# Performance work log

Measured on AMD Instinct MI355X. Metric: run time of the kernel, lower is better.

Reference implementation:

```python
import jax, jax.numpy as jnp
import numpy as np

N, C, H, W = 4, 128, 64, 64


def setup_inputs() -> dict:
    key = jax.random.key(0)
    ks = jax.random.split(key, 4)
    s = 1.0 / np.sqrt(C).astype(np.float32)  # conv2d default-init scale
    return {
        "x": jax.random.normal(ks[0], (N, C, H, W), dtype=jnp.float32),
        "Wq": jax.random.normal(ks[1], (C, C), dtype=jnp.float32) * s,
        "bq": jnp.zeros((C,), dtype=jnp.float32),
        "Wk": jax.random.normal(ks[2], (C, C), dtype=jnp.float32) * s,
        "bk": jnp.zeros((C,), dtype=jnp.float32),
        "Wv": jax.random.normal(ks[3], (C, C), dtype=jnp.float32) * s,
        "bv": jnp.zeros((C,), dtype=jnp.float32),
    }


def reference(x, Wq, bq, Wk, bk, Wv, bv):
    n, c, h, w = x.shape
    xf = x.reshape(n, c, h * w)  # [N, C, L], L = H*W
    # 1x1 convs == per-pixel channel mixing
    q = jnp.einsum('oc,ncl->nol', Wq, xf) + bq[:, None]
    k = jnp.einsum('oc,ncl->nol', Wk, xf) + bk[:, None]
    v = jnp.einsum('oc,ncl->nol', Wv, xf) + bv[:, None]
    # scores[l, m] = sum_c k[c,l] * q[c,m]  (matmul(k^T, q))
    scale = jnp.asarray(1.0 / np.sqrt(c), x.dtype)
    scores = jnp.einsum('ncl,ncm->nlm', k, q) * scale  # [N, L, L]
    temp = jax.nn.softmax(scores, axis=-1)
    attn = jnp.einsum('ncl,nlm->ncm', v, temp)  # [N, C, L]
    return x + attn.reshape(n, c, h, w)
```

## Files before the change

kernel.cpp:

```cpp
#include <hip/hip_runtime.h>
#include <hip/hip_bf16.h>
#include <stdint.h>

#define NB 4
#define CH 128
#define LL 4096

typedef __attribute__((ext_vector_type(8))) short short8;
typedef __attribute__((ext_vector_type(4))) short short4b;
typedef __attribute__((ext_vector_type(4))) float floatx4;
typedef __attribute__((ext_vector_type(16))) float floatx16;


static __device__ __forceinline__ short f2bf(float f) {
    uint32_t u = __float_as_uint(f);
    u += 0x7fffu + ((u >> 16) & 1u);
    return (short)(u >> 16);
}
static __device__ __forceinline__ float bf2f(short s) {
    return __uint_as_float(((uint32_t)(uint16_t)s) << 16);
}

__global__ __launch_bounds__(256) void wprep_kernel(
    const float* __restrict__ Wq, const float* __restrict__ Wk,
    const float* __restrict__ Wv, short* __restrict__ Wf)
{
    const int g = blockIdx.x * 256 + threadIdx.x;
    const int mat = g >> 14;
    const int rem = g & 16383;
    const int o   = rem >> 7;
    const int c   = rem & 127;
    const float* W = (mat == 0) ? Wq : (mat == 1) ? Wk : Wv;
    float v = W[o * CH + c];
    if (mat == 1) v *= 0.08838834764831845f;
    Wf[(size_t)mat * 16384 + (o >> 4) * 2048 + (c >> 5) * 512
       + ((c >> 3) & 3) * 128 + (o & 15) * 8 + (c & 7)] = f2bf(v);
}

__global__ __launch_bounds__(256) void proj_kernel(
    const float* __restrict__ x, const short* __restrict__ Wf,
    const float* __restrict__ bq, const float* __restrict__ bk,
    const float* __restrict__ bv,
    short* __restrict__ Qf, short* __restrict__ Kf, short* __restrict__ Vp)
{
    const int i    = blockIdx.x;
    const int n    = (i >> 1) & 3;
    const int lt   = ((i >> 3) << 1) | (i & 1);
    const int l0   = lt << 5;
    const int tid  = threadIdx.x;
    const int wave = tid >> 6;
    const int lane = tid & 63;
    const int quad = lane >> 4;
    const int mc   = lane & 15;

    __shared__ short Xb[32][136];

    {
        const int sl = tid & 31;
        const int cg = tid >> 5;
        const float* xp = x + ((size_t)n * CH + cg * 16) * LL + l0 + sl;
        short8 buf;
        #pragma unroll
        for (int i2 = 0; i2 < 16; ++i2) {
            buf[i2 & 7] = f2bf(xp[(size_t)i2 * LL]);
            if ((i2 & 7) == 7)
                *(short8*)(void*)&Xb[sl][cg * 16 + (i2 & 8)] = buf;
        }
    }
    __syncthreads();

    const int lt2 = wave >> 1;
    const int oh  = wave & 1;
    const int gt  = lt * 2 + lt2;

    short8 xf[4];
    #pragma unroll
    for (int s = 0; s < 4; ++s)
        xf[s] = *(const short8*)(const void*)&Xb[lt2 * 16 + mc][32 * s + quad * 8];

    const size_t obase = ((size_t)n * 256 + gt) * 2048;
    const float scale = 0.08838834764831845f;

    #pragma unroll
    for (int mat = 0; mat < 3; ++mat) {
        const short* Wm = Wf + (size_t)mat * 16384;
        const float* bb = (mat == 0) ? bq : (mat == 1) ? bk : bv;
        const float bscale = (mat == 1) ? scale : 1.0f;
        #pragma unroll
        for (int ot = oh * 4; ot < oh * 4 + 4; ++ot) {
            floatx4 acc = {0.f, 0.f, 0.f, 0.f};
            #pragma unroll
            for (int s = 0; s < 4; ++s)
                acc = __builtin_amdgcn_mfma_f32_16x16x32_bf16(
                    *(const short8*)(const void*)(Wm + ot * 2048 + s * 512 + lane * 8),
                    xf[s], acc, 0, 0, 0);
            const int c0 = ot * 16 + 4 * quad;
            if (mat < 2) {
                short4b pv;
                #pragma unroll
                for (int r = 0; r < 4; ++r)
                    pv[r] = f2bf(acc[r] + bb[c0 + r] * bscale);
                short* dst = ((mat == 0) ? Qf : Kf) + obase
                           + (c0 >> 5) * 512 + ((c0 >> 3) & 3) * 128
                           + mc * 8 + (c0 & 7);
                *(short4b*)(void*)dst = pv;
            } else {
                #pragma unroll
                for (int r = 0; r < 4; ++r)
                    Vp[obase + (c0 + r) * 16 + mc] = f2bf(acc[r] + bb[c0 + r]);
            }
        }
    }
}

__global__ __launch_bounds__(1024) void rowsum_kernel(
    const short* __restrict__ Qf, const short* __restrict__ Kf,
    float* __restrict__ Dv)
{
    const int i    = blockIdx.x;
    const int n    = (i >> 1) & 3;
    const int tq   = ((i >> 3) << 1) | (i & 1);
    const int tid  = threadIdx.x;
    const int wave = tid >> 6;
    const int lane = tid & 63;
    const int quad = lane >> 4;
    const int mc   = lane & 15;
    const int mw   = wave & 7;
    const int th   = wave >> 3;

    __shared__ float Db[16][32];

    const short* Kb = Kf + ((size_t)n * 256 + tq * 4 + th * 2) * 2048 + lane * 8;
    short8 kf[2][4];
    #pragma unroll
    for (int t = 0; t < 2; ++t)
        #pragma unroll
        for (int s = 0; s < 4; ++s)
            kf[t][s] = *(const short8*)(const void*)(Kb + t * 2048 + s * 512);

    const short* Qn = Qf + (size_t)n * 524288 + (size_t)mw * 32 * 2048 + lane * 8;
    float rs[2][4] = {{0.f, 0.f, 0.f, 0.f}, {0.f, 0.f, 0.f, 0.f}};

    for (int it = 0; it < 32; ++it) {
        short8 q[4];
        #pragma unroll
        for (int s = 0; s < 4; ++s)
            q[s] = *(const short8*)(const void*)(
                Qn + (size_t)it * 2048 + s * 512);
        floatx4 a0 = {0.f, 0.f, 0.f, 0.f};
        floatx4 a1 = {0.f, 0.f, 0.f, 0.f};
        #pragma unroll
        for (int s = 0; s < 4; ++s) {
            a0 = __builtin_amdgcn_mfma_f32_16x16x32_bf16(kf[0][s], q[s], a0, 0, 0, 0);
            a1 = __builtin_amdgcn_mfma_f32_16x16x32_bf16(kf[1][s], q[s], a1, 0, 0, 0);
        }
        #pragma unroll
        for (int r = 0; r < 4; ++r) {
            rs[0][r] += __expf(a0[r]);
            rs[1][r] += __expf(a1[r]);
        }
    }

    #pragma unroll
    for (int t = 0; t < 2; ++t)
        #pragma unroll
        for (int r = 0; r < 4; ++r) {
            float v = rs[t][r];
            v += __shfl_xor(v, 1);
            v += __shfl_xor(v, 2);
            v += __shfl_xor(v, 4);
            v += __shfl_xor(v, 8);
            if (mc == 0) Db[wave][t * 16 + quad * 4 + r] = v;
        }
    __syncthreads();
    if (tid < 64) {
        const int lh = tid >> 5, lr = tid & 31;
        float s = 0.f;
        #pragma unroll
        for (int m = 0; m < 8; ++m) s += Db[lh * 8 + m][lr];
        Dv[(size_t)n * 4096 + tq * 64 + tid] = 1.0f / s;
    }
}

__global__ __launch_bounds__(512, 4) void attn_out_kernel(
    const short* __restrict__ Qf, const short* __restrict__ Kf,
    const short* __restrict__ Vp, const float* __restrict__ Dv,
    float* __restrict__ Po)
{
    const int i    = blockIdx.x;
    const int n    = (i >> 1) & 3;
    const int j    = ((i >> 3) << 1) | (i & 1);
    const int lh   = j >> 6;
    const int mb   = j & 63;
    const int m0   = mb << 6;
    const int tid  = threadIdx.x;
    const int wave = tid >> 6;
    const int lane = tid & 63;
    const int quad = lane >> 4;
    const int mc   = lane & 15;
    const int l32  = lane & 31;
    const int h    = lane >> 5;
    const int ct   = wave & 3;
    const int mh   = wave >> 2;

    __shared__ short P[2][64][260];

    const short* Qn  = Qf + (size_t)n * 524288;
    const short* Kn  = Kf + (size_t)n * 524288;
    const short* Vpn = Vp + (size_t)n * 524288;
    const float* Dn  = Dv + (size_t)n * 4096;
    const int tile0  = lh * 128;

    floatx16 acc;
    #pragma unroll
    for (int r = 0; r < 16; ++r) acc[r] = 0.f;

    for (int t = 0; t < 8; ++t) {
        const int p = t & 1;

        {
            const int tb = tile0 + t * 16 + 2 * wave;
            short8 kfr[2][4];
            #pragma unroll
            for (int jj = 0; jj < 2; ++jj)
                #pragma unroll
                for (int s = 0; s < 4; ++s)
                    kfr[jj][s] = *(const short8*)(const void*)(
                        Kn + (size_t)(tb + jj) * 2048 + s * 512 + lane * 8);
            floatx4 dr[2];
            #pragma unroll
            for (int jj = 0; jj < 2; ++jj)
                dr[jj] = *(const floatx4*)(const void*)(
                    Dn + (tb + jj) * 16 + quad * 4);

            #pragma unroll
            for (int mst = 0; mst < 4; ++mst) {
                short8 qt[4];
                #pragma unroll
                for (int s = 0; s < 4; ++s)
                    qt[s] = *(const short8*)(const void*)(
                        Qn + (size_t)((m0 >> 4) + mst) * 2048 + s * 512 + lane * 8);
                floatx4 sa0 = {0.f, 0.f, 0.f, 0.f};
                floatx4 sa1 = {0.f, 0.f, 0.f, 0.f};
                #pragma unroll
                for (int s = 0; s < 4; ++s) {
                    sa0 = __builtin_amdgcn_mfma_f32_16x16x32_bf16(kfr[0][s], qt[s], sa0, 0, 0, 0);
                    sa1 = __builtin_amdgcn_mfma_f32_16x16x32_bf16(kfr[1][s], qt[s], sa1, 0, 0, 0);
                }
                short4b pv0, pv1;
                #pragma unroll
                for (int r = 0; r < 4; ++r) {
                    pv0[r] = f2bf(__expf(sa0[r]) * dr[0][r]);
                    pv1[r] = f2bf(__expf(sa1[r]) * dr[1][r]);
                }
                *(short4b*)(void*)&P[p][16 * mst + mc][32 * wave + quad * 4] = pv0;
                *(short4b*)(void*)&P[p][16 * mst + mc][32 * wave + 16 + quad * 4] = pv1;
            }
        }
        __syncthreads();

        #pragma unroll
        for (int kc = 0; kc < 16; ++kc) {
            const short8 vf = *(const short8*)(const void*)(
                Vpn + (size_t)(tile0 + t * 16 + kc) * 2048
                    + (32 * ct + l32) * 16 + 8 * h);
            const short8 pf = *(const short8*)(const void*)&P[p][32 * mh + l32][16 * kc + 8 * h];
            acc = __builtin_amdgcn_mfma_f32_32x32x16_bf16(vf, pf, acc, 0, 0, 0);
        }
    }

    float* Pon = Po + (size_t)(lh * 4 + n) * 524288;
    #pragma unroll
    for (int r = 0; r < 16; ++r) {
        const int c = 32 * ct + (r & 3) + 8 * (r >> 2) + 4 * h;
        const int m = m0 + 32 * mh + l32;
        Pon[(size_t)c * LL + m] = acc[r];
    }
}

__global__ __launch_bounds__(256) void combine_kernel(
    const float* __restrict__ x, const float* __restrict__ Po,
    float* __restrict__ out)
{
    const size_t k = (size_t)blockIdx.x * 256 + threadIdx.x;
    const floatx4 a = *(const floatx4*)(const void*)(x + 4 * k);
    const floatx4 b = *(const floatx4*)(const void*)(Po + 4 * k);
    const floatx4 c = *(const floatx4*)(const void*)(Po + 2097152 + 4 * k);
    floatx4 o;
    #pragma unroll
    for (int r = 0; r < 4; ++r) o[r] = a[r] + b[r] + c[r];
    *(floatx4*)(void*)(out + 4 * k) = o;
}

extern "C" void kernel_launch(void* const* d_in, const int* in_sizes, int n_in,
                              void* d_out, int out_size, void* d_ws, size_t ws_size,
                              hipStream_t stream) {
    (void)in_sizes; (void)n_in; (void)out_size; (void)ws_size;
    const float* x  = (const float*)d_in[0];
    const float* Wq = (const float*)d_in[1];
    const float* bq = (const float*)d_in[2];
    const float* Wk = (const float*)d_in[3];
    const float* bk = (const float*)d_in[4];
    const float* Wv = (const float*)d_in[5];
    const float* bv = (const float*)d_in[6];
    float* out = (float*)d_out;

    char* ws = (char*)d_ws;
    short* Qf = (short*)(ws);
    short* Kf = (short*)(ws + 4194304);
    short* Vp = (short*)(ws + 8388608);
    float* Dv = (float*)(ws + 12582912);
    short* Wf = (short*)(ws + 16777216);
    float* Po = (float*)(ws + 16908288);

    wprep_kernel<<<192, 256, 0, stream>>>(Wq, Wk, Wv, Wf);
    proj_kernel<<<512, 256, 0, stream>>>(x, Wf, bq, bk, bv, Qf, Kf, Vp);
    rowsum_kernel<<<256, 1024, 0, stream>>>(Qf, Kf, Dv);
    attn_out_kernel<<<512, 512, 0, stream>>>(Qf, Kf, Vp, Dv, Po);
    combine_kernel<<<2048, 256, 0, stream>>>(x, Po, out);
}
```

Before: 179.2 us.

## Fuse all stages into one cooperative persistent kernel with grid syncs

```diff
diff --git a/kernel.cpp b/kernel.cpp
--- a/kernel.cpp
+++ b/kernel.cpp
@@ -1,6 +1,9 @@
 #include <hip/hip_runtime.h>
 #include <hip/hip_bf16.h>
+#include <hip/hip_cooperative_groups.h>
 #include <stdint.h>
+
+namespace cg = cooperative_groups;
 
 #define NB 4
 #define CH 128
@@ -17,182 +20,26 @@
     u += 0x7fffu + ((u >> 16) & 1u);
     return (short)(u >> 16);
 }
-static __device__ __forceinline__ float bf2f(short s) {
-    return __uint_as_float(((uint32_t)(uint16_t)s) << 16);
-}
-
-__global__ __launch_bounds__(256) void wprep_kernel(
-    const float* __restrict__ Wq, const float* __restrict__ Wk,
-    const float* __restrict__ Wv, short* __restrict__ Wf)
+
+__global__ __launch_bounds__(1024) void mega_kernel(
+    const float* __restrict__ x,
+    const float* __restrict__ Wq, const float* __restrict__ bq,
+    const float* __restrict__ Wk, const float* __restrict__ bk,
+    const float* __restrict__ Wv, const float* __restrict__ bv,
+    short* __restrict__ Qf, short* __restrict__ Kf, short* __restrict__ Vp,
+    float* __restrict__ Dv, short* __restrict__ Wf,
+    float* __restrict__ out)
 {
-    const int g = blockIdx.x * 256 + threadIdx.x;
-    const int mat = g >> 14;
-    const int rem = g & 16383;
-    const int o   = rem >> 7;
-    const int c   = rem & 127;
-    const float* W = (mat == 0) ? Wq : (mat == 1) ? Wk : Wv;
-    float v = W[o * CH + c];
-    if (mat == 1) v *= 0.08838834764831845f;
-    Wf[(size_t)mat * 16384 + (o >> 4) * 2048 + (c >> 5) * 512
-       + ((c >> 3) & 3) * 128 + (o & 15) * 8 + (c & 7)] = f2bf(v);
-}
-
-__global__ __launch_bounds__(256) void proj_kernel(
-    const float* __restrict__ x, const short* __restrict__ Wf,
-    const float* __restrict__ bq, const float* __restrict__ bk,
-    const float* __restrict__ bv,
-    short* __restrict__ Qf, short* __restrict__ Kf, short* __restrict__ Vp)
-{
-    const int i    = blockIdx.x;
-    const int n    = (i >> 1) & 3;
-    const int lt   = ((i >> 3) << 1) | (i & 1);
-    const int l0   = lt << 5;
-    const int tid  = threadIdx.x;
-    const int wave = tid >> 6;
-    const int lane = tid & 63;
-    const int quad = lane >> 4;
-    const int mc   = lane & 15;
-
-    __shared__ short Xb[32][136];
-
-    {
-        const int sl = tid & 31;
-        const int cg = tid >> 5;
-        const float* xp = x + ((size_t)n * CH + cg * 16) * LL + l0 + sl;
-        short8 buf;
-        #pragma unroll
-        for (int i2 = 0; i2 < 16; ++i2) {
-            buf[i2 & 7] = f2bf(xp[(size_t)i2 * LL]);
-            if ((i2 & 7) == 7)
-                *(short8*)(void*)&Xb[sl][cg * 16 + (i2 & 8)] = buf;
-        }
-    }
-    __syncthreads();
-
-    const int lt2 = wave >> 1;
-    const int oh  = wave & 1;
-    const int gt  = lt * 2 + lt2;
-
-    short8 xf[4];
-    #pragma unroll
-    for (int s = 0; s < 4; ++s)
-        xf[s] = *(const short8*)(const void*)&Xb[lt2 * 16 + mc][32 * s + quad * 8];
-
-    const size_t obase = ((size_t)n * 256 + gt) * 2048;
-    const float scale = 0.08838834764831845f;
-
-    #pragma unroll
-    for (int mat = 0; mat < 3; ++mat) {
-        const short* Wm = Wf + (size_t)mat * 16384;
-        const float* bb = (mat == 0) ? bq : (mat == 1) ? bk : bv;
-        const float bscale = (mat == 1) ? scale : 1.0f;
-        #pragma unroll
-        for (int ot = oh * 4; ot < oh * 4 + 4; ++ot) {
-            floatx4 acc = {0.f, 0.f, 0.f, 0.f};
-            #pragma unroll
-            for (int s = 0; s < 4; ++s)
-                acc = __builtin_amdgcn_mfma_f32_16x16x32_bf16(
-                    *(const short8*)(const void*)(Wm + ot * 2048 + s * 512 + lane * 8),
-                    xf[s], acc, 0, 0, 0);
-            const int c0 = ot * 16 + 4 * quad;
-            if (mat < 2) {
-                short4b pv;
-                #pragma unroll
-                for (int r = 0; r < 4; ++r)
-                    pv[r] = f2bf(acc[r] + bb[c0 + r] * bscale);
-                short* dst = ((mat == 0) ? Qf : Kf) + obase
-                           + (c0 >> 5) * 512 + ((c0 >> 3) & 3) * 128
-                           + mc * 8 + (c0 & 7);
-                *(short4b*)(void*)dst = pv;
-            } else {
-                #pragma unroll
-                for (int r = 0; r < 4; ++r)
-                    Vp[obase + (c0 + r) * 16 + mc] = f2bf(acc[r] + bb[c0 + r]);
-            }
-        }
-    }
-}
-
-__global__ __launch_bounds__(1024) void rowsum_kernel(
-    const short* __restrict__ Qf, const short* __restrict__ Kf,
-    float* __restrict__ Dv)
-{
-    const int i    = blockIdx.x;
-    const int n    = (i >> 1) & 3;
-    const int tq   = ((i >> 3) << 1) | (i & 1);
-    const int tid  = threadIdx.x;
-    const int wave = tid >> 6;
-    const int lane = tid & 63;
-    const int quad = lane >> 4;
-    const int mc   = lane & 15;
-    const int mw   = wave & 7;
-    const int th   = wave >> 3;
-
-    __shared__ float Db[16][32];
-
-    const short* Kb = Kf + ((size_t)n * 256 + tq * 4 + th * 2) * 2048 + lane * 8;
-    short8 kf[2][4];
-    #pragma unroll
-    for (int t = 0; t < 2; ++t)
-        #pragma unroll
-        for (int s = 0; s < 4; ++s)
-            kf[t][s] = *(const short8*)(const void*)(Kb + t * 2048 + s * 512);
-
-    const short* Qn = Qf + (size_t)n * 524288 + (size_t)mw * 32 * 2048 + lane * 8;
-    float rs[2][4] = {{0.f, 0.f, 0.f, 0.f}, {0.f, 0.f, 0.f, 0.f}};
-
-    for (int it = 0; it < 32; ++it) {
-        short8 q[4];
-        #pragma unroll
-        for (int s = 0; s < 4; ++s)
-            q[s] = *(const short8*)(const void*)(
-                Qn + (size_t)it * 2048 + s * 512);
-        floatx4 a0 = {0.f, 0.f, 0.f, 0.f};
-        floatx4 a1 = {0.f, 0.f, 0.f, 0.f};
-        #pragma unroll
-        for (int s = 0; s < 4; ++s) {
-            a0 = __builtin_amdgcn_mfma_f32_16x16x32_bf16(kf[0][s], q[s], a0, 0, 0, 0);
-            a1 = __builtin_amdgcn_mfma_f32_16x16x32_bf16(kf[1][s], q[s], a1, 0, 0, 0);
-        }
-        #pragma unroll
-        for (int r = 0; r < 4; ++r) {
-            rs[0][r] += __expf(a0[r]);
-            rs[1][r] += __expf(a1[r]);
-        }
-    }
-
-    #pragma unroll
-    for (int t = 0; t < 2; ++t)
-        #pragma unroll
-        for (int r = 0; r < 4; ++r) {
-            float v = rs[t][r];
-            v += __shfl_xor(v, 1);
-            v += __shfl_xor(v, 2);
-            v += __shfl_xor(v, 4);
-            v += __shfl_xor(v, 8);
-            if (mc == 0) Db[wave][t * 16 + quad * 4 + r] = v;
-        }
-    __syncthreads();
-    if (tid < 64) {
-        const int lh = tid >> 5, lr = tid & 31;
-        float s = 0.f;
-        #pragma unroll
-        for (int m = 0; m < 8; ++m) s += Db[lh * 8 + m][lr];
-        Dv[(size_t)n * 4096 + tq * 64 + tid] = 1.0f / s;
-    }
-}
-
-__global__ __launch_bounds__(512, 4) void attn_out_kernel(
-    const short* __restrict__ Qf, const short* __restrict__ Kf,
-    const short* __restrict__ Vp, const float* __restrict__ Dv,
-    float* __restrict__ Po)
-{
-    const int i    = blockIdx.x;
-    const int n    = (i >> 1) & 3;
-    const int j    = ((i >> 3) << 1) | (i & 1);
-    const int lh   = j >> 6;
-    const int mb   = j & 63;
-    const int m0   = mb << 6;
+    cg::grid_group grid = cg::this_grid();
+
+    __shared__ union SH {
+        short P2[2][2][64][264];
+        short Xb[4][16][136];
+        float Db[16][32];
+        float Rb[8192];
+    } sh;
+
+    const int ib   = blockIdx.x;
     const int tid  = threadIdx.x;
     const int wave = tid >> 6;
     const int lane = tid & 63;
@@ -200,96 +47,235 @@
     const int mc   = lane & 15;
     const int l32  = lane & 31;
     const int h    = lane >> 5;
-    const int ct   = wave & 3;
-    const int mh   = wave >> 2;
-
-    __shared__ short P[2][64][260];
-
-    const short* Qn  = Qf + (size_t)n * 524288;
-    const short* Kn  = Kf + (size_t)n * 524288;
-    const short* Vpn = Vp + (size_t)n * 524288;
-    const float* Dn  = Dv + (size_t)n * 4096;
-    const int tile0  = lh * 128;
-
-    floatx16 acc;
-    #pragma unroll
-    for (int r = 0; r < 16; ++r) acc[r] = 0.f;
-
-    for (int t = 0; t < 8; ++t) {
-        const int p = t & 1;
+
+    const int n   = (ib >> 1) & 3;
+    const int b64 = ((ib >> 3) << 1) | (ib & 1);
+
+    {
+        const int g = ib * 1024 + tid;
+        if (g < 49152) {
+            const int mat = g >> 14;
+            const int rem = g & 16383;
+            const int o   = rem >> 7;
+            const int c   = rem & 127;
+            const float* W = (mat == 0) ? Wq : (mat == 1) ? Wk : Wv;
+            float v = W[o * CH + c];
+            if (mat == 1) v *= 0.08838834764831845f;
+            Wf[(size_t)mat * 16384 + (o >> 4) * 2048 + (c >> 5) * 512
+               + ((c >> 3) & 3) * 128 + (o & 15) * 8 + (c & 7)] = f2bf(v);
+        }
+    }
+    grid.sync();
+
+    {
+        const int sub  = tid >> 8;
+        const int stid = tid & 255;
+        const int gt   = b64 * 4 + sub;
+        const int l0   = gt << 4;
+        const int w4   = (tid >> 6) & 3;
 
         {
-            const int tb = tile0 + t * 16 + 2 * wave;
-            short8 kfr[2][4];
-            #pragma unroll
-            for (int jj = 0; jj < 2; ++jj)
+            const int sl = stid & 15;
+            const int cg = stid >> 4;
+            const float* xp = x + ((size_t)n * CH + cg * 8) * LL + l0 + sl;
+            short8 buf;
+            #pragma unroll
+            for (int i2 = 0; i2 < 8; ++i2)
+                buf[i2] = f2bf(xp[(size_t)i2 * LL]);
+            *(short8*)(void*)&sh.Xb[sub][sl][cg * 8] = buf;
+        }
+        __syncthreads();
+
+        short8 xf[4];
+        #pragma unroll
+        for (int s = 0; s < 4; ++s)
+            xf[s] = *(const short8*)(const void*)&sh.Xb[sub][mc][32 * s + quad * 8];
+
+        const size_t obase = ((size_t)n * 256 + gt) * 2048;
+        const float scale = 0.08838834764831845f;
+
+        #pragma unroll
+        for (int mat = 0; mat < 3; ++mat) {
+            const short* Wm = Wf + (size_t)mat * 16384;
+            const float* bb = (mat == 0) ? bq : (mat == 1) ? bk : bv;
+            const float bscale = (mat == 1) ? scale : 1.0f;
+            #pragma unroll
+            for (int oo = 0; oo < 2; ++oo) {
+                const int ot = w4 * 2 + oo;
+                floatx4 acc = {0.f, 0.f, 0.f, 0.f};
                 #pragma unroll
                 for (int s = 0; s < 4; ++s)
-                    kfr[jj][s] = *(const short8*)(const void*)(
-                        Kn + (size_t)(tb + jj) * 2048 + s * 512 + lane * 8);
-            floatx4 dr[2];
-            #pragma unroll
-            for (int jj = 0; jj < 2; ++jj)
-                dr[jj] = *(const floatx4*)(const void*)(
-                    Dn + (tb + jj) * 16 + quad * 4);
-
-            #pragma unroll
-            for (int mst = 0; mst < 4; ++mst) {
-                short8 qt[4];
+                    acc = __builtin_amdgcn_mfma_f32_16x16x32_bf16(
+                        *(const short8*)(const void*)(Wm + ot * 2048 + s * 512 + lane * 8),
+                        xf[s], acc, 0, 0, 0);
+                const int c0 = ot * 16 + 4 * quad;
+                if (mat < 2) {
+                    short4b pv;
+                    #pragma unroll
+                    for (int r = 0; r < 4; ++r)
+                        pv[r] = f2bf(acc[r] + bb[c0 + r] * bscale);
+                    short* dst = ((mat == 0) ? Qf : Kf) + obase
+                               + (c0 >> 5) * 512 + ((c0 >> 3) & 3) * 128
+                               + mc * 8 + (c0 & 7);
+                    *(short4b*)(void*)dst = pv;
+                } else {
+                    #pragma unroll
+                    for (int r = 0; r < 4; ++r)
+                        Vp[obase + (c0 + r) * 16 + mc] = f2bf(acc[r] + bb[c0 + r]);
+                }
+            }
+        }
+    }
+    grid.sync();
+
+    {
+        const int tq = b64;
+        const int mw = wave & 7;
+        const int th = wave >> 3;
+
+        const short* Kb = Kf + ((size_t)n * 256 + tq * 4 + th * 2) * 2048 + lane * 8;
+        short8 kf[2][4];
+        #pragma unroll
+        for (int t = 0; t < 2; ++t)
+            #pragma unroll
+            for (int s = 0; s < 4; ++s)
+                kf[t][s] = *(const short8*)(const void*)(Kb + t * 2048 + s * 512);
+
+        const short* Qn = Qf + (size_t)n * 524288 + (size_t)mw * 32 * 2048 + lane * 8;
+        float rs[2][4] = {{0.f, 0.f, 0.f, 0.f}, {0.f, 0.f, 0.f, 0.f}};
+
+        for (int it = 0; it < 32; ++it) {
+            short8 q[4];
+            #pragma unroll
+            for (int s = 0; s < 4; ++s)
+                q[s] = *(const short8*)(const void*)(Qn + (size_t)it * 2048 + s * 512);
+            floatx4 a0 = {0.f, 0.f, 0.f, 0.f};
+            floatx4 a1 = {0.f, 0.f, 0.f, 0.f};
+            #pragma unroll
+            for (int s = 0; s < 4; ++s) {
+                a0 = __builtin_amdgcn_mfma_f32_16x16x32_bf16(kf[0][s], q[s], a0, 0, 0, 0);
+                a1 = __builtin_amdgcn_mfma_f32_16x16x32_bf16(kf[1][s], q[s], a1, 0, 0, 0);
+            }
+            #pragma unroll
+            for (int r = 0; r < 4; ++r) {
+                rs[0][r] += __expf(a0[r]);
+                rs[1][r] += __expf(a1[r]);
+            }
+        }
+
+        __syncthreads();
+        #pragma unroll
+        for (int t = 0; t < 2; ++t)
+            #pragma unroll
+            for (int r = 0; r < 4; ++r) {
+                float v = rs[t][r];
+                v += __shfl_xor(v, 1);
+                v += __shfl_xor(v, 2);
+                v += __shfl_xor(v, 4);
+                v += __shfl_xor(v, 8);
+                if (mc == 0) sh.Db[wave][t * 16 + quad * 4 + r] = v;
+            }
+        __syncthreads();
+        if (tid < 64) {
+            const int lhh = tid >> 5, lr = tid & 31;
+            float s = 0.f;
+            #pragma unroll
+            for (int m = 0; m < 8; ++m) s += sh.Db[lhh * 8 + m][lr];
+            Dv[(size_t)n * 4096 + tq * 64 + tid] = 1.0f / s;
+        }
+    }
+    grid.sync();
+
+    {
+        const int mb  = b64;
+        const int m0  = mb << 6;
+        const int w8  = wave & 7;
+        const int lh  = wave >> 3;
+        const int ct  = w8 & 3;
+        const int mh  = w8 >> 2;
+
+        const short* Qn  = Qf + (size_t)n * 524288;
+        const short* Kn  = Kf + (size_t)n * 524288;
+        const short* Vpn = Vp + (size_t)n * 524288;
+        const float* Dn  = Dv + (size_t)n * 4096;
+        const int tile0  = lh * 128;
+
+        floatx16 acc;
+        #pragma unroll
+        for (int r = 0; r < 16; ++r) acc[r] = 0.f;
+
+        for (int t = 0; t < 8; ++t) {
+            const int p   = t & 1;
+            const int tb0 = tile0 + t * 16;
+
+            {
+                const int tb = tb0 + 2 * w8;
+                short8 kfr[2][4];
                 #pragma unroll
-                for (int s = 0; s < 4; ++s)
-                    qt[s] = *(const short8*)(const void*)(
-                        Qn + (size_t)((m0 >> 4) + mst) * 2048 + s * 512 + lane * 8);
-                floatx4 sa0 = {0.f, 0.f, 0.f, 0.f};
-                floatx4 sa1 = {0.f, 0.f, 0.f, 0.f};
+                for (int jj = 0; jj < 2; ++jj)
+                    #pragma unroll
+                    for (int s = 0; s < 4; ++s)
+                        kfr[jj][s] = *(const short8*)(const void*)(
+                            Kn + (size_t)(tb + jj) * 2048 + s * 512 + lane * 8);
+                floatx4 dr[2];
                 #pragma unroll
-                for (int s = 0; s < 4; ++s) {
-                    sa0 = __builtin_amdgcn_mfma_f32_16x16x32_bf16(kfr[0][s], qt[s], sa0, 0, 0, 0);
-                    sa1 = __builtin_amdgcn_mfma_f32_16x16x32_bf16(kfr[1][s], qt[s], sa1, 0, 0, 0);
+                for (int jj = 0; jj < 2; ++jj)
+                    dr[jj] = *(const floatx4*)(const void*)(
+                        Dn + (tb + jj) * 16 + quad * 4);
+
+                #pragma unroll
+                for (int mst = 0; mst < 4; ++mst) {
+                    short8 qt[4];
+                    #pragma unroll
+                    for (int s = 0; s < 4; ++s)
+                        qt[s] = *(const short8*)(const void*)(
+                            Qn + (size_t)((m0 >> 4) + mst) * 2048 + s * 512 + lane * 8);
+                    floatx4 sa0 = {0.f, 0.f, 0.f, 0.f};
+                    floatx4 sa1 = {0.f, 0.f, 0.f, 0.f};
+                    #pragma unroll
+                    for (int s = 0; s < 4; ++s) {
+                        sa0 = __builtin_amdgcn_mfma_f32_16x16x32_bf16(kfr[0][s], qt[s], sa0, 0, 0, 0);
+                        sa1 = __builtin_amdgcn_mfma_f32_16x16x32_bf16(kfr[1][s], qt[s], sa1, 0, 0, 0);
+                    }
+                    short4b pv0, pv1;
+                    #pragma unroll
+                    for (int r = 0; r < 4; ++r) {
+                        pv0[r] = f2bf(__expf(sa0[r]) * dr[0][r]);
+                        pv1[r] = f2bf(__expf(sa1[r]) * dr[1][r]);
+                    }
+                    *(short4b*)(void*)&sh.P2[lh][p][16 * mst + mc][32 * w8 + quad * 4] = pv0;
+                    *(short4b*)(void*)&sh.P2[lh][p][16 * mst + mc][32 * w8 + 16 + quad * 4] = pv1;
                 }
-                short4b pv0, pv1;
-                #pragma unroll
-                for (int r = 0; r < 4; ++r) {
-                    pv0[r] = f2bf(__expf(sa0[r]) * dr[0][r]);
-                    pv1[r] = f2bf(__expf(sa1[r]) * dr[1][r]);
-                }
-                *(short4b*)(void*)&P[p][16 * mst + mc][32 * wave + quad * 4] = pv0;
-                *(short4b*)(void*)&P[p][16 * mst + mc][32 * wave + 16 + quad * 4] = pv1;
-            }
-        }
-        __syncthreads();
-
-        #pragma unroll
-        for (int kc = 0; kc < 16; ++kc) {
-            const short8 vf = *(const short8*)(const void*)(
-                Vpn + (size_t)(tile0 + t * 16 + kc) * 2048
-                    + (32 * ct + l32) * 16 + 8 * h);
-            const short8 pf = *(const short8*)(const void*)&P[p][32 * mh + l32][16 * kc + 8 * h];
-            acc = __builtin_amdgcn_mfma_f32_32x32x16_bf16(vf, pf, acc, 0, 0, 0);
+            }
+            __syncthreads();
+
+            #pragma unroll
+            for (int kc = 0; kc < 16; ++kc) {
+                const short8 vf = *(const short8*)(const void*)(
+                    Vpn + (size_t)(tb0 + kc) * 2048
+                        + (32 * ct + l32) * 16 + 8 * h);
+                const short8 pf = *(const short8*)(const void*)
+                    &sh.P2[lh][p][32 * mh + l32][16 * kc + 8 * h];
+                acc = __builtin_amdgcn_mfma_f32_32x32x16_bf16(vf, pf, acc, 0, 0, 0);
+            }
+        }
+
+        __syncthreads();
+        if (lh == 1)
+            *(floatx16*)(void*)&sh.Rb[(w8 * 64 + lane) * 16] = acc;
+        __syncthreads();
+        if (lh == 0) {
+            const floatx16 o = *(const floatx16*)(const void*)
+                &sh.Rb[(w8 * 64 + lane) * 16];
+            #pragma unroll
+            for (int r = 0; r < 16; ++r) {
+                const int c = 32 * ct + (r & 3) + 8 * (r >> 2) + 4 * h;
+                const int m = m0 + 32 * mh + l32;
+                const size_t idx = ((size_t)n * CH + c) * LL + m;
+                out[idx] = x[idx] + acc[r] + o[r];
+            }
         }
     }
-
-    float* Pon = Po + (size_t)(lh * 4 + n) * 524288;
-    #pragma unroll
-    for (int r = 0; r < 16; ++r) {
-        const int c = 32 * ct + (r & 3) + 8 * (r >> 2) + 4 * h;
-        const int m = m0 + 32 * mh + l32;
-        Pon[(size_t)c * LL + m] = acc[r];
-    }
-}
-
-__global__ __launch_bounds__(256) void combine_kernel(
-    const float* __restrict__ x, const float* __restrict__ Po,
-    float* __restrict__ out)
-{
-    const size_t k = (size_t)blockIdx.x * 256 + threadIdx.x;
-    const floatx4 a = *(const floatx4*)(const void*)(x + 4 * k);
-    const floatx4 b = *(const floatx4*)(const void*)(Po + 4 * k);
-    const floatx4 c = *(const floatx4*)(const void*)(Po + 2097152 + 4 * k);
-    floatx4 o;
-    #pragma unroll
-    for (int r = 0; r < 4; ++r) o[r] = a[r] + b[r] + c[r];
-    *(floatx4*)(void*)(out + 4 * k) = o;
 }
 
 extern "C" void kernel_launch(void* const* d_in, const int* in_sizes, int n_in,
@@ -311,11 +297,12 @@
     short* Vp = (short*)(ws + 8388608);
     float* Dv = (float*)(ws + 12582912);
     short* Wf = (short*)(ws + 16777216);
-    float* Po = (float*)(ws + 16908288);
-
-    wprep_kernel<<<192, 256, 0, stream>>>(Wq, Wk, Wv, Wf);
-    proj_kernel<<<512, 256, 0, stream>>>(x, Wf, bq, bk, bv, Qf, Kf, Vp);
-    rowsum_kernel<<<256, 1024, 0, stream>>>(Qf, Kf, Dv);
-    attn_out_kernel<<<512, 512, 0, stream>>>(Qf, Kf, Vp, Dv, Po);
-    combine_kernel<<<2048, 256, 0, stream>>>(x, Po, out);
+
+    void* args[] = {
+        (void*)&x, (void*)&Wq, (void*)&bq, (void*)&Wk, (void*)&bk,
+        (void*)&Wv, (void*)&bv, (void*)&Qf, (void*)&Kf, (void*)&Vp,
+        (void*)&Dv, (void*)&Wf, (void*)&out
+    };
+    hipLaunchCooperativeKernel((const void*)mega_kernel,
+                               dim3(256), dim3(1024), args, 0, stream);
 }
```

Result: slower. 247.7 us (+38.2%).
